# Performance work log

Hardware: AMD Instinct MI355X
Metric: run time of the kernel (lower is better)

## Reference

```python
import jax, jax.numpy as jnp
import numpy as np

B, S, HID = 2, 2048, 2048
H, HKV, D = 16, 8, 128
RQ, RK, RV = 6, 2, 2
WINDOW = 1024
SOFTCAP = 50.0
SCALING = D ** -0.5
NEG_INF = -2.3819763e38  # gemma mask fill value (fp32 safe)


def _rope(x, cos, sin):
    # Gemma rotary: split last dim into two halves treated as (real, imag).
    d2 = x.shape[-1] // 2
    x1, x2 = x[..., :d2], x[..., d2:]
    return jnp.concatenate([x1 * cos - x2 * sin, x1 * sin + x2 * cos], axis=-1)


def setup_inputs() -> dict:
    key = jax.random.key(0)
    ks = jax.random.split(key, 8)
    hidden_states = jax.random.normal(ks[0], (B, S, HID), jnp.float32)
    w = 0.02
    W_A_q = jax.random.normal(ks[1], (HID, H * RQ), jnp.float32) * w
    W_B_q = jax.random.normal(ks[2], (HID, H * RQ * D), jnp.float32) * w
    W_A_k = jax.random.normal(ks[3], (HID, HKV * RK), jnp.float32) * w
    W_B_k = jax.random.normal(ks[4], (HID, RK * D), jnp.float32) * w
    W_A_v = jax.random.normal(ks[5], (HID, HKV * RV), jnp.float32) * w
    W_B_v = jax.random.normal(ks[6], (HID, RV * D), jnp.float32) * w
    W_o = jax.random.normal(ks[7], (H * D, HID), jnp.float32) * w
    # rotary tables (theta=10000)
    pos = jnp.arange(S, dtype=jnp.float32)
    inv = 1.0 / (10000.0 ** (jnp.arange(0, D, 2, dtype=jnp.float32) / D))
    ang = pos[:, None] * inv[None, :]  # [S, D/2]
    freqs_cos, freqs_sin = jnp.cos(ang), jnp.sin(ang)
    # causal + sliding-window additive mask [B,1,S,S]
    i = jnp.arange(S)[:, None]
    j = jnp.arange(S)[None, :]
    allowed = (j <= i) & (i - j < WINDOW)
    mask = jnp.where(allowed, 0.0, NEG_INF).astype(jnp.float32)
    mask = jnp.broadcast_to(mask[None, None], (B, 1, S, S))
    kv_write_indices = jnp.arange(S, dtype=jnp.int32)  # prefill: identity write
    return {
        'hidden_states': hidden_states, 'W_A_q': W_A_q, 'W_B_q': W_B_q,
        'W_A_k': W_A_k, 'W_B_k': W_B_k, 'W_A_v': W_A_v, 'W_B_v': W_B_v,
        'W_o': W_o, 'freqs_cos': freqs_cos, 'freqs_sin': freqs_sin,
        'mask': mask, 'kv_write_indices': kv_write_indices,
    }


def reference(hidden_states, W_A_q, W_B_q, W_A_k, W_B_k, W_A_v, W_B_v, W_o,
              freqs_cos, freqs_sin, mask, kv_write_indices):
    # Prefill: kv_write_indices == arange(S); factorized cache == current factors.
    b, s, _ = hidden_states.shape
    Aq = (hidden_states @ W_A_q).reshape(b, s, H, RQ)       # [b,s,H,Rq]
    Bq = (hidden_states @ W_B_q).reshape(b, s, H, RQ, D)    # [b,s,H,Rq,d]
    Ak = (hidden_states @ W_A_k).reshape(b, s, HKV, RK)
    Bk = (hidden_states @ W_B_k).reshape(b, s, RK, D)
    Av = (hidden_states @ W_A_v).reshape(b, s, HKV, RV)
    Bv = (hidden_states @ W_B_v).reshape(b, s, RV, D)
    # RoPE on the B factors (as in the original: applied to B_q rows and B_k rows)
    Bq = _rope(Bq, freqs_cos[:, None, None, :], freqs_sin[:, None, None, :])
    Bk = _rope(Bk, freqs_cos[:, None, :], freqs_sin[:, None, :])
    # Contract rank factors. Identical math to the per-head
    # einsum('bqrd,bksd->bqkrs') + einsum('bqr,bks,bqkrs->bqk') since the
    # bilinear form factorizes: sum_{r,s} Aq_r Ak_s <Bq_r, Bk_s> = <q, k>.
    q = jnp.einsum('bshr,bshrd->bshd', Aq, Bq)               # [b,s,H,d]
    k = jnp.einsum('bsgr,bsrd->bsgd', Ak, Bk)                # [b,s,Hkv,d]
    v = jnp.einsum('bsgr,bsrd->bsgd', Av, Bv)
    rep = H // HKV
    k = jnp.repeat(k, rep, axis=2)                            # GQA expand
    v = jnp.repeat(v, rep, axis=2)
    scores = jnp.einsum('bqhd,bkhd->bhqk', q, k) * SCALING
    scores = jnp.tanh(scores / SOFTCAP) * SOFTCAP             # logit softcap
    scores = scores + mask                                    # local sliding mask
    probs = jax.nn.softmax(scores, axis=-1)
    out = jnp.einsum('bhqk,bkhd->bqhd', probs, v).reshape(b, s, H * D)
    return out @ W_o
```

## Files before the change

### kernel.cpp

```cpp
#include <hip/hip_runtime.h>
#include <hip/hip_bf16.h>

#define S_LEN 2048
#define HID 2048
#define NB 2
#define NH 16
#define NKV 8
#define DH 128
#define RQ 6
#define KG 2048
#define SCALING 0.08838834764831845f

typedef __attribute__((ext_vector_type(8))) short s16x8;
typedef __attribute__((ext_vector_type(4))) float f32x4;

__device__ __forceinline__ float bf2f(ushort u) {
    union { unsigned int i; float f; } v; v.i = ((unsigned int)u) << 16; return v.f;
}
__device__ __forceinline__ ushort f2bf(float f) {
    __hip_bfloat16 h = __float2bfloat16(f);
    return *reinterpret_cast<ushort*>(&h);
}
__device__ __forceinline__ void g2lds16(const void* g, void* l) {
    __builtin_amdgcn_global_load_lds((const __attribute__((address_space(1))) void*)g,
                                     (__attribute__((address_space(3))) void*)l, 16, 0, 0);
}

__global__ void k_prep(const float* __restrict__ hs, const float* __restrict__ WAq,
                       const float* __restrict__ WAk, const float* __restrict__ WAv,
                       const float* __restrict__ WBk, const float* __restrict__ WBv,
                       const float* __restrict__ WBq, const float* __restrict__ Wo,
                       ushort* __restrict__ Xb, ushort* __restrict__ WtS,
                       ushort* __restrict__ WtBq, ushort* __restrict__ WtWo) {
    __shared__ ushort tile[64][68];
    int idx = blockIdx.x;
    int t = threadIdx.x;
    if (idx < 2048) {
#pragma unroll
        for (int j = 0; j < 4; ++j) {
            int i = idx * 1024 + t + j * 256;
            float4 v = ((const float4*)hs)[i];
            ushort4 o;
            o.x = f2bf(v.x); o.y = f2bf(v.y); o.z = f2bf(v.z); o.w = f2bf(v.w);
            ((ushort4*)Xb)[i] = o;
        }
        return;
    }
    idx -= 2048;
    const float* in; ushort* out; int Nin, rowOff;
    if (idx < 64)        { in = WAq; out = WtS;  Nin = 96;    rowOff = 0; }
    else if (idx < 96)   { idx -= 64;   in = WAk; out = WtS;  Nin = 16;    rowOff = 96; }
    else if (idx < 128)  { idx -= 96;   in = WAv; out = WtS;  Nin = 16;    rowOff = 112; }
    else if (idx < 256)  { idx -= 128;  in = WBk; out = WtS;  Nin = 256;   rowOff = 128; }
    else if (idx < 384)  { idx -= 256;  in = WBv; out = WtS;  Nin = 256;   rowOff = 384; }
    else if (idx < 6528) { idx -= 384;  in = WBq; out = WtBq; Nin = 12288; rowOff = 0; }
    else                 { idx -= 6528; in = Wo;  out = WtWo; Nin = 2048;  rowOff = 0; }
    int k0 = (idx & 31) * 64, n0 = (idx >> 5) * 64;
#pragma unroll
    for (int i = 0; i < 4; ++i) {
        int f = t + i * 256;
        int r = f >> 4;
        int c = (f & 15) * 4;
        int nn = n0 + c;
        float4 v = make_float4(0.f, 0.f, 0.f, 0.f);
        if (nn < Nin) v = *(const float4*)&in[(size_t)(k0 + r) * Nin + nn];
        ushort4 u;
        u.x = f2bf(v.x); u.y = f2bf(v.y); u.z = f2bf(v.z); u.w = f2bf(v.w);
        *(ushort4*)&tile[r][c] = u;
    }
    __syncthreads();
#pragma unroll
    for (int i = 0; i < 4; ++i) {
        int f = t + i * 256;
        int nr = f >> 4;
        int kc = (f & 15) * 4;
        int nn = n0 + nr;
        if (nn < Nin) {
            ushort4 u;
            u.x = tile[kc][nr]; u.y = tile[kc + 1][nr];
            u.z = tile[kc + 2][nr]; u.w = tile[kc + 3][nr];
            *(ushort4*)&out[(size_t)(rowOff + nn) * KG + k0 + kc] = u;
        }
    }
}

__device__ __forceinline__ void stc(float* p, float v) { *p = v; }
__device__ __forceinline__ void stc(ushort* p, float v) { *p = f2bf(v); }

template<typename OutT>
__global__ __launch_bounds__(256, 2) void k_gemm(const ushort* __restrict__ A,
                                                 const ushort* __restrict__ Bt,
                                                 OutT* __restrict__ C, int ldc) {
    __shared__ ushort lA[128 * 64];
    __shared__ ushort lB[128 * 64];
    const int tid = threadIdx.x;
    const int l = tid & 63, w = tid >> 6;
    const int gx = gridDim.x;
    int flat = blockIdx.y * gx + blockIdx.x;
    const int nwg = gx * gridDim.y;
    if ((nwg & 7) == 0) {
        int qq = nwg >> 3;
        flat = (flat & 7) * qq + (flat >> 3);
    }
    const int m0 = (flat % gx) * 128, n0 = (flat / gx) * 128;
    const int wm = w >> 1, wn = w & 1;
    f32x4 acc[4][4] = {};
    const int swz = 16 * ((tid & 7) ^ ((tid >> 3) & 7));
    const int rowbase = tid >> 3;

    for (int k0 = 0; k0 < KG; k0 += 64) {
#pragma unroll
        for (int i = 0; i < 4; ++i) {
            int row = rowbase + i * 32;
            const char* srcA = (const char*)A + (((size_t)(m0 + row) * KG + k0) * 2) + swz;
            g2lds16(srcA, (char*)lA + tid * 16 + i * 4096);
            const char* srcB = (const char*)Bt + (((size_t)(n0 + row) * KG + k0) * 2) + swz;
            g2lds16(srcB, (char*)lB + tid * 16 + i * 4096);
        }
        __syncthreads();
#pragma unroll
        for (int kk = 0; kk < 2; ++kk) {
            s16x8 af[4], bfr[4];
            const int kb = kk * 64 + (l >> 4) * 16;
#pragma unroll
            for (int mf = 0; mf < 4; ++mf) {
                int row = wm * 64 + mf * 16 + (l & 15);
                af[mf] = *(const s16x8*)((const char*)lA + row * 128 + (kb ^ ((row & 7) << 4)));
            }
#pragma unroll
            for (int nf = 0; nf < 4; ++nf) {
                int row = wn * 64 + nf * 16 + (l & 15);
                bfr[nf] = *(const s16x8*)((const char*)lB + row * 128 + (kb ^ ((row & 7) << 4)));
            }
#pragma unroll
            for (int mf = 0; mf < 4; ++mf)
#pragma unroll
                for (int nf = 0; nf < 4; ++nf)
                    acc[mf][nf] = __builtin_amdgcn_mfma_f32_16x16x32_bf16(af[mf], bfr[nf], acc[mf][nf], 0, 0, 0);
        }
        __syncthreads();
    }
#pragma unroll
    for (int mf = 0; mf < 4; ++mf)
#pragma unroll
        for (int r = 0; r < 4; ++r) {
            int row = m0 + wm * 64 + mf * 16 + (l >> 4) * 4 + r;
#pragma unroll
            for (int nf = 0; nf < 4; ++nf) {
                int col = n0 + wn * 64 + nf * 16 + (l & 15);
                stc(C + (size_t)row * ldc + col, acc[mf][nf][r]);
            }
        }
}

__global__ __launch_bounds__(512, 2) void k_mega(const ushort* __restrict__ Xb,
                                                 const ushort* __restrict__ WtBq,
                                                 ushort* __restrict__ BqC,
                                                 const ushort* __restrict__ WtS,
                                                 float* __restrict__ Small) {
    __shared__ char sB[131072];
    const int tid = threadIdx.x;
    const int l = tid & 63, wid = tid >> 6;

    if (blockIdx.x < 768) {
        const ushort* A = Xb;
        const ushort* Bt = WtBq;
        ushort* C = BqC;
        const int ldc = 12288;
        const int wr = wid >> 2, wc = wid & 3;

        int flat = blockIdx.x;
        {
            int qq = 768 >> 3;
            flat = (flat & 7) * qq + (flat >> 3);
        }
        const int m0 = (flat & 15) * 256;
        const int n0 = (flat >> 4) * 256;

        const int rb = tid >> 3;
        const int swz = 16 * ((tid & 7) ^ (rb & 7));
        const char* pAh[2][2];
        const char* pBh[2][2];
#pragma unroll
        for (int h = 0; h < 2; ++h)
#pragma unroll
            for (int j = 0; j < 2; ++j) {
                pAh[h][j] = (const char*)A + (size_t)(m0 + j * 128 + h * 64 + rb) * (KG * 2) + swz;
                pBh[h][j] = (const char*)Bt + (size_t)(n0 + (j * 2 + (tid >> 8)) * 64 + h * 32 + (rb & 31)) * (KG * 2) + swz;
            }

        f32x4 acc[8][4] = {};
        s16x8 af[4][2], bf[4][2];

        const int arow = (l & 15) * 128;
        const int kxor0 = (0 * 64 + (l >> 4) * 16) ^ ((l & 7) << 4);
        const int kxor1 = (1 * 64 + (l >> 4) * 16) ^ ((l & 7) << 4);

#define STG_A(T, D, H)                                                                     \
    do {                                                                                   \
        g2lds16(pAh[H][0] + (size_t)(T) * 128, sB + (D) * 65536 + (H) * 16384 + tid * 16); \
        g2lds16(pAh[H][1] + (size_t)(T) * 128, sB + (D) * 65536 + (H) * 16384 + 8192 + tid * 16); \
    } while (0)
#define STG_B(T, D, H)                                                                     \
    do {                                                                                   \
        g2lds16(pBh[H][0] + (size_t)(T) * 128, sB + (D) * 65536 + 32768 + (H) * 16384 + tid * 16); \
        g2lds16(pBh[H][1] + (size_t)(T) * 128, sB + (D) * 65536 + 32768 + (H) * 16384 + 8192 + tid * 16); \
    } while (0)
#define RD_A(D, MH)                                                                        \
    do {                                                                                   \
        const char* ab = sB + (D) * 65536 + (MH) * 16384 + wr * 8192;                      \
        _Pragma("unroll") for (int mi = 0; mi < 4; ++mi) {                                 \
            af[mi][0] = *(const s16x8*)(ab + mi * 2048 + arow + kxor0);                    \
            af[mi][1] = *(const s16x8*)(ab + mi * 2048 + arow + kxor1);                    \
        }                                                                                  \
    } while (0)
#define RD_B(D, BH)                                                                        \
    do {                                                                                   \
        const char* bb = sB + (D) * 65536 + 32768 + (BH) * 16384 + wc * 4096;              \
        _Pragma("unroll") for (int ni = 0; ni < 2; ++ni) {                                 \
            bf[(BH) * 2 + ni][0] = *(const s16x8*)(bb + ni * 2048 + arow + kxor0);         \
            bf[(BH) * 2 + ni][1] = *(const s16x8*)(bb + ni * 2048 + arow + kxor1);         \
        }                                                                                  \
    } while (0)
#define QMFMA(MQ, NQ)                                                                      \
    do {                                                                                   \
        __builtin_amdgcn_s_setprio(1);                                                     \
        _Pragma("unroll") for (int mi = 0; mi < 4; ++mi)                                   \
        _Pragma("unroll") for (int ni = 0; ni < 2; ++ni)                                   \
        _Pragma("unroll") for (int k2 = 0; k2 < 2; ++k2)                                   \
            acc[(MQ) * 4 + mi][(NQ) * 2 + ni] = __builtin_amdgcn_mfma_f32_16x16x32_bf16(   \
                af[mi][k2], bf[(NQ) * 2 + ni][k2], acc[(MQ) * 4 + mi][(NQ) * 2 + ni], 0, 0, 0); \
        __builtin_amdgcn_s_setprio(0);                                                     \
    } while (0)
#define BAR()                                   \
    do {                                        \
        asm volatile("" ::: "memory");          \
        __builtin_amdgcn_s_barrier();           \
        asm volatile("" ::: "memory");          \
    } while (0)
#define VM6() asm volatile("s_waitcnt vmcnt(6)" ::: "memory")
#define VM0() asm volatile("s_waitcnt vmcnt(0)" ::: "memory")

        STG_A(0, 0, 0); STG_A(0, 0, 1); STG_B(0, 0, 0); STG_B(0, 0, 1);
        STG_B(1, 1, 0); STG_B(1, 1, 1); STG_A(1, 1, 0);
        VM6();
        BAR();

        for (int i = 0; i < 16; ++i) {
            const bool last = (i == 15);
            const int t1 = 2 * i + 1, t2 = 2 * i + 2, t3 = 2 * i + 3;
            RD_A(0, 0); RD_B(0, 0);
            STG_A(t1, 1, 1);
            BAR(); QMFMA(0, 0); BAR();
            RD_B(0, 1);
            if (!last) STG_A(t2, 0, 0);
            BAR(); QMFMA(0, 1); BAR();
            RD_A(0, 1);
            if (!last) STG_B(t2, 0, 0);
            BAR(); QMFMA(1, 1); BAR();
            if (!last) { STG_B(t2, 0, 1); VM6(); } else { VM0(); }
            BAR(); QMFMA(1, 0); BAR();
            RD_A(1, 0); RD_B(1, 0);
            if (!last) STG_A(t2, 0, 1);
            BAR(); QMFMA(0, 0); BAR();
            RD_B(1, 1);
            if (!last) STG_B(t3, 1, 0);
            BAR(); QMFMA(0, 1); BAR();
            RD_A(1, 1);
            if (!last) STG_B(t3, 1, 1);
            BAR(); QMFMA(1, 1); BAR();
            if (!last) { STG_A(t3, 1, 0); VM6(); }
            BAR(); QMFMA(1, 0); BAR();
        }

#undef STG_A
#undef STG_B
#undef RD_A
#undef RD_B
#undef QMFMA
#undef BAR
#undef VM6
#undef VM0

#pragma unroll
        for (int mf = 0; mf < 8; ++mf)
#pragma unroll
            for (int r = 0; r < 4; ++r) {
                int row = m0 + wr * 128 + mf * 16 + (l >> 4) * 4 + r;
#pragma unroll
                for (int nf = 0; nf < 4; ++nf) {
                    int col = n0 + wc * 64 + nf * 16 + (l & 15);
                    C[(size_t)row * ldc + col] = f2bf(acc[mf][nf][r]);
                }
            }
    } else {
        ushort* lA = (ushort*)sB;
        ushort* lB = (ushort*)(sB + 16384);
        int flat = blockIdx.x - 768;
        {
            int qq = 160 >> 3;
            flat = (flat & 7) * qq + (flat >> 3);
        }
        const int m0 = (flat % 32) * 128, n0 = (flat / 32) * 128;
        const int w = wid;
        const int wm = (w & 3) >> 1, wn = w & 1;
        f32x4 acc[4][4] = {};
        const int swz = 16 * ((tid & 7) ^ ((tid >> 3) & 7));
        const int rowbase = tid >> 3;

        for (int k0 = 0; k0 < KG; k0 += 64) {
#pragma unroll
            for (int i = 0; i < 2; ++i) {
                int row = rowbase + i * 64;
                const char* srcA = (const char*)Xb + (((size_t)(m0 + row) * KG + k0) * 2) + swz;
                g2lds16(srcA, (char*)lA + tid * 16 + i * 8192);
                const char* srcB = (const char*)WtS + (((size_t)(n0 + row) * KG + k0) * 2) + swz;
                g2lds16(srcB, (char*)lB + tid * 16 + i * 8192);
            }
            __syncthreads();
            if (w < 4) {
#pragma unroll
                for (int kk = 0; kk < 2; ++kk) {
                    s16x8 af[4], bfr[4];
                    const int kb = kk * 64 + (l >> 4) * 16;
#pragma unroll
                    for (int mf = 0; mf < 4; ++mf) {
                        int row = wm * 64 + mf * 16 + (l & 15);
                        af[mf] = *(const s16x8*)((const char*)lA + row * 128 + (kb ^ ((row & 7) << 4)));
                    }
#pragma unroll
                    for (int nf = 0; nf < 4; ++nf) {
                        int row = wn * 64 + nf * 16 + (l & 15);
                        bfr[nf] = *(const s16x8*)((const char*)lB + row * 128 + (kb ^ ((row & 7) << 4)));
                    }
#pragma unroll
                    for (int mf = 0; mf < 4; ++mf)
#pragma unroll
                        for (int nf = 0; nf < 4; ++nf)
                            acc[mf][nf] = __builtin_amdgcn_mfma_f32_16x16x32_bf16(af[mf], bfr[nf], acc[mf][nf], 0, 0, 0);
                }
            }
            __syncthreads();
        }
        if (w < 4) {
#pragma unroll
            for (int mf = 0; mf < 4; ++mf)
#pragma unroll
                for (int r = 0; r < 4; ++r) {
                    int row = m0 + wm * 64 + mf * 16 + (l >> 4) * 4 + r;
#pragma unroll
                    for (int nf = 0; nf < 4; ++nf) {
                        int col = n0 + wn * 64 + nf * 16 + (l & 15);
                        Small[(size_t)row * 640 + col] = acc[mf][nf][r];
                    }
                }
        }
    }
}

__global__ __launch_bounds__(512, 2) void k_gemm8(const ushort* __restrict__ A,
                                                  const ushort* __restrict__ Bt,
                                                  ushort* __restrict__ C, int ldc) {
    __shared__ char sB[131072];
    const int tid = threadIdx.x;
    const int l = tid & 63, wid = tid >> 6;
    const int wr = wid >> 2, wc = wid & 3;

    int flat = blockIdx.x;
    const int nwg = gridDim.x;
    if ((nwg & 7) == 0) {
        int qq = nwg >> 3;
        flat = (flat & 7) * qq + (flat >> 3);
    }
    const int m0 = (flat & 15) * 256;
    const int n0 = (flat >> 4) * 256;

    const int rb = tid >> 3;
    const int swz = 16 * ((tid & 7) ^ (rb & 7));
    const char* pAh[2][2];
    const char* pBh[2][2];
#pragma unroll
    for (int h = 0; h < 2; ++h)
#pragma unroll
        for (int j = 0; j < 2; ++j) {
            pAh[h][j] = (const char*)A + (size_t)(m0 + j * 128 + h * 64 + rb) * (KG * 2) + swz;
            pBh[h][j] = (const char*)Bt + (size_t)(n0 + (j * 2 + (tid >> 8)) * 64 + h * 32 + (rb & 31)) * (KG * 2) + swz;
        }

    f32x4 acc[8][4] = {};
    s16x8 af[4][2], bf[4][2];

    const int arow = (l & 15) * 128;
    const int kxor0 = (0 * 64 + (l >> 4) * 16) ^ ((l & 7) << 4);
    const int kxor1 = (1 * 64 + (l >> 4) * 16) ^ ((l & 7) << 4);

#define STG_A(T, D, H)                                                                     \
    do {                                                                                   \
        g2lds16(pAh[H][0] + (size_t)(T) * 128, sB + (D) * 65536 + (H) * 16384 + tid * 16); \
        g2lds16(pAh[H][1] + (size_t)(T) * 128, sB + (D) * 65536 + (H) * 16384 + 8192 + tid * 16); \
    } while (0)
#define STG_B(T, D, H)                                                                     \
    do {                                                                                   \
        g2lds16(pBh[H][0] + (size_t)(T) * 128, sB + (D) * 65536 + 32768 + (H) * 16384 + tid * 16); \
        g2lds16(pBh[H][1] + (size_t)(T) * 128, sB + (D) * 65536 + 32768 + (H) * 16384 + 8192 + tid * 16); \
    } while (0)
#define RD_A(D, MH)                                                                        \
    do {                                                                                   \
        const char* ab = sB + (D) * 65536 + (MH) * 16384 + wr * 8192;                      \
        _Pragma("unroll") for (int mi = 0; mi < 4; ++mi) {                                 \
            af[mi][0] = *(const s16x8*)(ab + mi * 2048 + arow + kxor0);                    \
            af[mi][1] = *(const s16x8*)(ab + mi * 2048 + arow + kxor1);                    \
        }                                                                                  \
    } while (0)
#define RD_B(D, BH)                                                                        \
    do {                                                                                   \
        const char* bb = sB + (D) * 65536 + 32768 + (BH) * 16384 + wc * 4096;              \
        _Pragma("unroll") for (int ni = 0; ni < 2; ++ni) {                                 \
            bf[(BH) * 2 + ni][0] = *(const s16x8*)(bb + ni * 2048 + arow + kxor0);         \
            bf[(BH) * 2 + ni][1] = *(const s16x8*)(bb + ni * 2048 + arow + kxor1);         \
        }                                                                                  \
    } while (0)
#define QMFMA(MQ, NQ)                                                                      \
    do {                                                                                   \
        __builtin_amdgcn_s_setprio(1);                                                     \
        _Pragma("unroll") for (int mi = 0; mi < 4; ++mi)                                   \
        _Pragma("unroll") for (int ni = 0; ni < 2; ++ni)                                   \
        _Pragma("unroll") for (int k2 = 0; k2 < 2; ++k2)                                   \
            acc[(MQ) * 4 + mi][(NQ) * 2 + ni] = __builtin_amdgcn_mfma_f32_16x16x32_bf16(   \
                af[mi][k2], bf[(NQ) * 2 + ni][k2], acc[(MQ) * 4 + mi][(NQ) * 2 + ni], 0, 0, 0); \
        __builtin_amdgcn_s_setprio(0);                                                     \
    } while (0)
#define BAR()                                   \
    do {                                        \
        asm volatile("" ::: "memory");          \
        __builtin_amdgcn_s_barrier();           \
        asm volatile("" ::: "memory");          \
    } while (0)
#define VM6() asm volatile("s_waitcnt vmcnt(6)" ::: "memory")
#define VM0() asm volatile("s_waitcnt vmcnt(0)" ::: "memory")

    STG_A(0, 0, 0); STG_A(0, 0, 1); STG_B(0, 0, 0); STG_B(0, 0, 1);
    STG_B(1, 1, 0); STG_B(1, 1, 1); STG_A(1, 1, 0);
    VM6();
    BAR();

    for (int i = 0; i < 16; ++i) {
        const bool last = (i == 15);
        const int t1 = 2 * i + 1, t2 = 2 * i + 2, t3 = 2 * i + 3;
        RD_A(0, 0); RD_B(0, 0);
        STG_A(t1, 1, 1);
        BAR(); QMFMA(0, 0); BAR();
        RD_B(0, 1);
        if (!last) STG_A(t2, 0, 0);
        BAR(); QMFMA(0, 1); BAR();
        RD_A(0, 1);
        if (!last) STG_B(t2, 0, 0);
        BAR(); QMFMA(1, 1); BAR();
        if (!last) { STG_B(t2, 0, 1); VM6(); } else { VM0(); }
        BAR(); QMFMA(1, 0); BAR();
        RD_A(1, 0); RD_B(1, 0);
        if (!last) STG_A(t2, 0, 1);
        BAR(); QMFMA(0, 0); BAR();
        RD_B(1, 1);
        if (!last) STG_B(t3, 1, 0);
        BAR(); QMFMA(0, 1); BAR();
        RD_A(1, 1);
        if (!last) STG_B(t3, 1, 1);
        BAR(); QMFMA(1, 1); BAR();
        if (!last) { STG_A(t3, 1, 0); VM6(); }
        BAR(); QMFMA(1, 0); BAR();
    }

#undef STG_A
#undef STG_B
#undef RD_A
#undef RD_B
#undef QMFMA

#pragma unroll
    for (int mf = 0; mf < 8; ++mf)
#pragma unroll
        for (int r = 0; r < 4; ++r) {
            int row = m0 + wr * 128 + mf * 16 + (l >> 4) * 4 + r;
#pragma unroll
            for (int nf = 0; nf < 4; ++nf) {
                int col = n0 + wc * 64 + nf * 16 + (l & 15);
                C[(size_t)row * ldc + col] = f2bf(acc[mf][nf][r]);
            }
        }
#undef BAR
#undef VM6
#undef VM0
}

__global__ __launch_bounds__(512, 2) void k_gemm8h(const ushort* __restrict__ A,
                                                   const ushort* __restrict__ Bt,
                                                   float* __restrict__ C, int ldc) {
    __shared__ char sB[98304];
    const int tid = threadIdx.x;
    const int l = tid & 63, wid = tid >> 6;
    const int wr = wid >> 2, wc = wid & 3;

    int flat = blockIdx.x;
    const int nwg = gridDim.x;
    if ((nwg & 7) == 0) {
        int qq = nwg >> 3;
        flat = (flat & 7) * qq + (flat >> 3);
    }
    const int m0 = (flat & 31) * 128;
    const int n0 = (flat >> 5) * 256;

    const int rb = tid >> 3;
    const int swz = 16 * ((tid & 7) ^ (rb & 7));
    const char* pA_[2];
    const char* pB_[2][2];
#pragma unroll
    for (int h = 0; h < 2; ++h) {
        pA_[h] = (const char*)A + (size_t)(m0 + (tid >> 8) * 64 + h * 32 + (rb & 31)) * (KG * 2) + swz;
#pragma unroll
        for (int j = 0; j < 2; ++j)
            pB_[h][j] = (const char*)Bt + (size_t)(n0 + (j * 2 + (tid >> 8)) * 64 + h * 32 + (rb & 31)) * (KG * 2) + swz;
    }

    f32x4 acc[4][4] = {};
    s16x8 af[2][2], bf[4][2];

    const int arow = (l & 15) * 128;
    const int kxor0 = ((l >> 4) * 16) ^ ((l & 7) << 4);
    const int kxor1 = (64 + (l >> 4) * 16) ^ ((l & 7) << 4);

#define STG_AH(T, D, H)                                                                    \
    g2lds16(pA_[H] + (size_t)(T) * 128, sB + (D) * 49152 + (H) * 8192 + tid * 16)
#define STG_BH(T, D, H)                                                                    \
    do {                                                                                   \
        g2lds16(pB_[H][0] + (size_t)(T) * 128, sB + (D) * 49152 + 16384 + (H) * 16384 + tid * 16); \
        g2lds16(pB_[H][1] + (size_t)(T) * 128, sB + (D) * 49152 + 16384 + (H) * 16384 + 8192 + tid * 16); \
    } while (0)
#define RD_AH(D, MH)                                                                       \
    do {                                                                                   \
        const char* ab = sB + (D) * 49152 + (MH) * 8192 + wr * 4096;                       \
        _Pragma("unroll") for (int mi = 0; mi < 2; ++mi) {                                 \
            af[mi][0] = *(const s16x8*)(ab + mi * 2048 + arow + kxor0);                    \
            af[mi][1] = *(const s16x8*)(ab + mi * 2048 + arow + kxor1);                    \
        }                                                                                  \
    } while (0)
#define RD_BH(D, BH)                                                                       \
    do {                                                                                   \
        const char* bb = sB + (D) * 49152 + 16384 + (BH) * 16384 + wc * 4096;              \
        _Pragma("unroll") for (int ni = 0; ni < 2; ++ni) {                                 \
            bf[(BH) * 2 + ni][0] = *(const s16x8*)(bb + ni * 2048 + arow + kxor0);         \
            bf[(BH) * 2 + ni][1] = *(const s16x8*)(bb + ni * 2048 + arow + kxor1);         \
        }                                                                                  \
    } while (0)
#define QMFMAH(MQ, NQ)                                                                     \
    do {                                                                                   \
        __builtin_amdgcn_s_setprio(1);                                                     \
        _Pragma("unroll") for (int mi = 0; mi < 2; ++mi)                                   \
        _Pragma("unroll") for (int ni = 0; ni < 2; ++ni)                                   \
        _Pragma("unroll") for (int k2 = 0; k2 < 2; ++k2)                                   \
            acc[(MQ) * 2 + mi][(NQ) * 2 + ni] = __builtin_amdgcn_mfma_f32_16x16x32_bf16(   \
                af[mi][k2], bf[(NQ) * 2 + ni][k2], acc[(MQ) * 2 + mi][(NQ) * 2 + ni], 0, 0, 0); \
        __builtin_amdgcn_s_setprio(0);                                                     \
    } while (0)
#define BAR()                                   \
    do {                                        \
        asm volatile("" ::: "memory");          \
        __builtin_amdgcn_s_barrier();           \
        asm volatile("" ::: "memory");          \
    } while (0)
#define VM5() asm volatile("s_waitcnt vmcnt(5)" ::: "memory")
#define VM0() asm volatile("s_waitcnt vmcnt(0)" ::: "memory")

    STG_AH(0, 0, 0); STG_AH(0, 0, 1); STG_BH(0, 0, 0); STG_BH(0, 0, 1);
    STG_BH(1, 1, 0); STG_BH(1, 1, 1); STG_AH(1, 1, 0);
    VM5();
    BAR();

    for (int i = 0; i < 16; ++i) {
        const bool last = (i == 15);
        const int t1 = 2 * i + 1, t2 = 2 * i + 2, t3 = 2 * i + 3;
        RD_AH(0, 0); RD_BH(0, 0);
        STG_AH(t1, 1, 1);
        BAR(); QMFMAH(0, 0); BAR();
        RD_BH(0, 1);
        if (!last) STG_AH(t2, 0, 0);
        BAR(); QMFMAH(0, 1); BAR();
        RD_AH(0, 1);
        if (!last) STG_BH(t2, 0, 0);
        BAR(); QMFMAH(1, 1); BAR();
        if (!last) { STG_BH(t2, 0, 1); VM5(); } else { VM0(); }
        BAR(); QMFMAH(1, 0); BAR();
        RD_AH(1, 0); RD_BH(1, 0);
        if (!last) STG_AH(t2, 0, 1);
        BAR(); QMFMAH(0, 0); BAR();
        RD_BH(1, 1);
        if (!last) STG_BH(t3, 1, 0);
        BAR(); QMFMAH(0, 1); BAR();
        RD_AH(1, 1);
        if (!last) STG_BH(t3, 1, 1);
        BAR(); QMFMAH(1, 1); BAR();
        if (!last) { STG_AH(t3, 1, 0); VM5(); }
        BAR(); QMFMAH(1, 0); BAR();
    }

#undef STG_AH
#undef STG_BH
#undef RD_AH
#undef RD_BH
#undef QMFMAH
#undef BAR
#undef VM5
#undef VM0

#pragma unroll
    for (int a = 0; a < 4; ++a)
#pragma unroll
        for (int r = 0; r < 4; ++r) {
            int row = m0 + wr * 64 + a * 16 + (l >> 4) * 4 + r;
#pragma unroll
            for (int b2 = 0; b2 < 4; ++b2) {
                int col = n0 + wc * 64 + b2 * 16 + (l & 15);
                C[(size_t)row * ldc + col] = acc[a][b2][r];
            }
        }
}

__global__ void k_contract_q(const ushort* __restrict__ bq, const float* __restrict__ small,
                             const float* __restrict__ cosT, const float* __restrict__ sinT,
                             ushort* __restrict__ q, int pitch, int hbase) {
    int srow = blockIdx.x;
    int b = srow >> 11, sl = srow & 2047;
    int t = threadIdx.x;
    int l = t & 63;
    int hloc = blockIdx.y * 4 + (t >> 6);
    int h = hbase + hloc;
    const ushort* bqr = bq + (size_t)srow * pitch + hloc * 768;
    const float* af = small + (size_t)srow * 640 + h * RQ;
    float y0 = 0.f, y1 = 0.f;
#pragma unroll
    for (int r = 0; r < RQ; ++r) {
        float a = af[r];
        ushort2 v = *(const ushort2*)&bqr[r * 128 + 2 * l];
        y0 += a * bf2f(v.x);
        y1 += a * bf2f(v.y);
    }
    float z0 = __shfl_xor(y0, 32);
    float z1 = __shfl_xor(y1, 32);
    int d = (l & 31) * 2;
    float2 cs = *(const float2*)&cosT[sl * 64 + d];
    float2 sn = *(const float2*)&sinT[sl * 64 + d];
    size_t o = ((size_t)(b * NH + h) * S_LEN + sl) * DH;
    ushort2 outv;
    if (l < 32) {
        outv.x = f2bf((y0 * cs.x - z0 * sn.x) * SCALING);
        outv.y = f2bf((y1 * cs.y - z1 * sn.y) * SCALING);
        *(ushort2*)&q[o + d] = outv;
    } else {
        outv.x = f2bf((z0 * sn.x + y0 * cs.x) * SCALING);
        outv.y = f2bf((z1 * sn.y + y1 * cs.y) * SCALING);
        *(ushort2*)&q[o + 64 + d] = outv;
    }
}

__global__ void k_contract_kv(const float* __restrict__ small, const float* __restrict__ cosT,
                              const float* __restrict__ sinT, ushort* __restrict__ kk,
                              ushort* __restrict__ vT) {
    int srow = blockIdx.x;
    int b = srow >> 11, sl = srow & 2047;
    int t = threadIdx.x;
    int d2 = t & 63, g = t >> 6;
    const float* row = small + (size_t)srow * 640;
    float k1 = 0.f, k2 = 0.f, v1 = 0.f, v2 = 0.f;
#pragma unroll
    for (int r = 0; r < 2; ++r) {
        float ak = row[96 + g * 2 + r];
        k1 += ak * row[128 + r * 128 + d2];
        k2 += ak * row[128 + r * 128 + 64 + d2];
        float av = row[112 + g * 2 + r];
        v1 += av * row[384 + r * 128 + d2];
        v2 += av * row[384 + r * 128 + 64 + d2];
    }
    float c = cosT[sl * 64 + d2], s = sinT[sl * 64 + d2];
    float kr1 = k1 * c - k2 * s, kr2 = k1 * s + k2 * c;
    size_t ko = ((size_t)(b * NKV + g) * S_LEN + sl) * DH + d2;
    kk[ko] = f2bf(kr1);
    kk[ko + 64] = f2bf(kr2);
    size_t vo = ((size_t)(b * NKV + g) * DH + d2) * S_LEN + sl;
    vT[vo] = f2bf(v1);
    vT[vo + (size_t)64 * S_LEN] = f2bf(v2);
}

__device__ __forceinline__ float softcap_p(float x) {
    float z = x * 0.02f;
    float z2 = z * z;
    float num = z * fmaf(z2, z2 + 105.f, 945.f);
    float den = fmaf(z2, fmaf(z2, 15.f, 420.f), 945.f);
    return __expf(fmaf(50.f, __fdividef(num, den), -50.f));
}

template<int FUSEQ>
__global__ __launch_bounds__(512, 2) void k_attn(const ushort* __restrict__ qsrc,
                                                 const float* __restrict__ small,
                                                 const float* __restrict__ cosT,
                                                 const float* __restrict__ sinT,
                                                 const ushort* __restrict__ kk,
                                                 const ushort* __restrict__ vT,
                                                 ushort* __restrict__ O) {
    __shared__ char sK[2][16384];
    __shared__ char sV[2][16384];
    __shared__ char sP[16384];
    const int f = blockIdx.x;
    const int xcd = f & 7;
    const int j = f >> 3;
    const int bg = xcd * 2 + (j >> 5);
    const int qb = 31 - (j & 31);
    const int b = bg >> 3, g = bg & 7;
    const int tid = threadIdx.x, l = tid & 63, w = tid >> 6;
    const int w4 = w & 3;
    const int h = g * 2 + (w >> 2);
    const int qs = qb * 64;
    const int q0 = qs + w4 * 16;

    s16x8 qf[4];
    if (FUSEQ) {
        const int row = q0 + (l & 15);
        const int srow = b * S_LEN + row;
        const float* af = small + (size_t)srow * 640 + h * RQ;
        const ushort* bqr = qsrc + (size_t)srow * 12288 + h * 768;
        const int k8 = (l >> 4) * 8;
#pragma unroll
        for (int grp = 0; grp < 2; ++grp) {
            const int dbase = grp * 32 + k8;
            float x1[8] = {}, x2[8] = {};
#pragma unroll
            for (int r = 0; r < RQ; ++r) {
                float a = af[r];
                s16x8 v1 = *(const s16x8*)&bqr[r * 128 + dbase];
                s16x8 v2 = *(const s16x8*)&bqr[r * 128 + 64 + dbase];
#pragma unroll
                for (int e = 0; e < 8; ++e) {
                    x1[e] = fmaf(a, bf2f((ushort)v1[e]), x1[e]);
                    x2[e] = fmaf(a, bf2f((ushort)v2[e]), x2[e]);
                }
            }
            const float* cp = &cosT[row * 64 + dbase];
            const float* sp = &sinT[row * 64 + dbase];
            s16x8 lo, hi;
#pragma unroll
            for (int e = 0; e < 8; ++e) {
                float c = cp[e], s = sp[e];
                lo[e] = (short)f2bf((x1[e] * c - x2[e] * s) * SCALING);
                hi[e] = (short)f2bf((x1[e] * s + x2[e] * c) * SCALING);
            }
            qf[grp] = lo;
            qf[grp + 2] = hi;
        }
    } else {
        const ushort* qbase = qsrc + ((size_t)(b * NH + h) * S_LEN) * DH;
        const char* qrow = (const char*)(qbase + (size_t)(q0 + (l & 15)) * DH);
#pragma unroll
        for (int ds = 0; ds < 4; ++ds)
            qf[ds] = *(const s16x8*)(qrow + ds * 64 + (l >> 4) * 16);
    }

    f32x4 acc[8] = {};
    float lrow[4] = {0.f, 0.f, 0.f, 0.f};

    const size_t kgbase = ((size_t)(b * NKV + g) * S_LEN) * DH * 2;
    const size_t vgbase = ((size_t)(b * NKV + g) * DH) * S_LEN * 2;

    const int jt0 = (qs > 1023) ? ((qs - 1023) >> 6) : 0;
    const int ibase = q0 + (l >> 4) * 4;

    const int krow0 = tid >> 4, kcolb = (tid & 15) * 16;
    const int vrow0 = tid >> 3, vcolb = (tid & 7) * 16;

#define STAGE_KV(JT, SLOT)                                                                   \
    do {                                                                                     \
        _Pragma("unroll")                                                                    \
        for (int i = 0; i < 2; ++i) {                                                        \
            int row = krow0 + i * 32;                                                        \
            const char* src = (const char*)kk + kgbase + ((size_t)((JT) * 64 + row)) * 256   \
                              + (kcolb ^ ((row & 7) << 4));                                  \
            g2lds16(src, &sK[SLOT][tid * 16 + i * 8192]);                                    \
        }                                                                                    \
        _Pragma("unroll")                                                                    \
        for (int i = 0; i < 2; ++i) {                                                        \
            int row = vrow0 + i * 64;                                                        \
            const char* src = (const char*)vT + vgbase + (size_t)row * 4096                  \
                              + (size_t)(JT) * 128 + (vcolb ^ ((row & 7) << 4));             \
            g2lds16(src, &sV[SLOT][tid * 16 + i * 8192]);                                    \
        }                                                                                    \
    } while (0)

    STAGE_KV(jt0, 0);
    asm volatile("s_waitcnt vmcnt(0)" ::: "memory");
    __builtin_amdgcn_s_barrier();
    asm volatile("" ::: "memory");

    for (int jt = jt0; jt <= qb; ++jt) {
        const int cur = (jt - jt0) & 1;
        if (jt < qb) STAGE_KV(jt + 1, cur ^ 1);

        const bool diag = (jt == qb);
        const bool wclip = (jt == jt0) && (qs > 1023);

        f32x4 sc[4] = {};
#pragma unroll
        for (int ct = 0; ct < 4; ++ct) {
            if (diag && ct > w4) continue;
            f32x4 z = {};
            int row = ct * 16 + (l & 15);
#pragma unroll
            for (int ds = 0; ds < 4; ++ds) {
                int kb = ds * 64 + (l >> 4) * 16;
                s16x8 kf = *(const s16x8*)(&sK[cur][row * 256 + (kb ^ ((row & 7) << 4))]);
                z = __builtin_amdgcn_mfma_f32_16x16x32_bf16(qf[ds], kf, z, 0, 0, 0);
            }
            sc[ct] = z;
        }
        float p[4][4];
        if (!diag && !wclip) {
#pragma unroll
            for (int ct = 0; ct < 4; ++ct)
#pragma unroll
                for (int r = 0; r < 4; ++r) {
                    float pe = softcap_p(sc[ct][r]);
                    p[ct][r] = pe;
                    lrow[r] += pe;
                }
        } else if (diag) {
#pragma unroll
            for (int ct = 0; ct < 4; ++ct) {
                if (ct > w4) {
#pragma unroll
                    for (int r = 0; r < 4; ++r) p[ct][r] = 0.f;
                    continue;
                }
                int j2 = jt * 64 + ct * 16 + (l & 15);
#pragma unroll
                for (int r = 0; r < 4; ++r) {
                    float pe = softcap_p(sc[ct][r]);
                    pe = (j2 <= ibase + r) ? pe : 0.f;
                    p[ct][r] = pe;
                    lrow[r] += pe;
                }
            }
        } else {
#pragma unroll
            for (int ct = 0; ct < 4; ++ct) {
                int j2 = jt * 64 + ct * 16 + (l & 15);
#pragma unroll
                for (int r = 0; r < 4; ++r) {
                    float pe = softcap_p(sc[ct][r]);
                    pe = (j2 > ibase + r - 1024) ? pe : 0.f;
                    p[ct][r] = pe;
                    lrow[r] += pe;
                }
            }
        }
#pragma unroll
        for (int ct = 0; ct < 4; ++ct) {
            int col = ct * 16 + (l & 15);
#pragma unroll
            for (int r = 0; r < 4; ++r) {
                int row = (l >> 4) * 4 + r;
                *(ushort*)(sP + w * 2048 + row * 128 + ((col * 2) ^ ((row & 7) << 4))) = f2bf(p[ct][r]);
            }
        }
#pragma unroll
        for (int s2 = 0; s2 < 2; ++s2) {
            int rowp = l & 15;
            int kb = s2 * 64 + (l >> 4) * 16;
            s16x8 pf = *(const s16x8*)(sP + w * 2048 + rowp * 128 + (kb ^ ((rowp & 7) << 4)));
#pragma unroll
            for (int dt = 0; dt < 8; ++dt) {
                int d = dt * 16 + (l & 15);
                s16x8 vf = *(const s16x8*)(&sV[cur][d * 128 + (kb ^ ((d & 7) << 4))]);
                acc[dt] = __builtin_amdgcn_mfma_f32_16x16x32_bf16(pf, vf, acc[dt], 0, 0, 0);
            }
        }

        asm volatile("s_waitcnt vmcnt(0)" ::: "memory");
        __builtin_amdgcn_s_barrier();
        asm volatile("" ::: "memory");
    }
#undef STAGE_KV

#pragma unroll
    for (int r = 0; r < 4; ++r) {
        float rs = lrow[r];
        rs += __shfl_xor(rs, 1); rs += __shfl_xor(rs, 2);
        rs += __shfl_xor(rs, 4); rs += __shfl_xor(rs, 8);
        lrow[r] = rs;
    }
#pragma unroll
    for (int r = 0; r < 4; ++r) {
        int row = qs + w4 * 16 + (l >> 4) * 4 + r;
        float inv = 1.f / lrow[r];
#pragma unroll
        for (int dt = 0; dt < 8; ++dt)
            O[((size_t)(b * S_LEN + row)) * HID + h * DH + dt * 16 + (l & 15)] = f2bf(acc[dt][r] * inv);
    }
}

extern "C" void kernel_launch(void* const* d_in, const int* in_sizes, int n_in,
                              void* d_out, int out_size, void* d_ws, size_t ws_size,
                              hipStream_t stream) {
    (void)in_sizes; (void)n_in; (void)out_size;
    const float* hs  = (const float*)d_in[0];
    const float* WAq = (const float*)d_in[1];
    const float* WBq = (const float*)d_in[2];
    const float* WAk = (const float*)d_in[3];
    const float* WBk = (const float*)d_in[4];
    const float* WAv = (const float*)d_in[5];
    const float* WBv = (const float*)d_in[6];
    const float* Wo  = (const float*)d_in[7];
    const float* fc  = (const float*)d_in[8];
    const float* fs  = (const float*)d_in[9];

    char* ws = (char*)d_ws;
    ushort* Xb    = (ushort*)(ws + 0);
    ushort* WtS   = (ushort*)(ws + 16777216);
    ushort* WtBq  = (ushort*)(ws + 19398656);
    ushort* WtWo  = (ushort*)(ws + 69730304);
    float*  Small = (float*) (ws + 78118912);
    ushort* BqC   = (ushort*)(ws + 88604672);

    const bool bigws = (ws_size >= 239599616ull);
    size_t tail = bigws ? 189267968ull : 113770496ull;
    ushort* qB  = (ushort*)(ws + tail);
    ushort* kB  = (ushort*)(ws + tail + 16777216);
    ushort* vTB = (ushort*)(ws + tail + 25165824);
    ushort* OB  = (ushort*)(ws + tail + 33554432);

    k_prep<<<9600, 256, 0, stream>>>(hs, WAq, WAk, WAv, WBk, WBv, WBq, Wo,
                                     Xb, WtS, WtBq, WtWo);

    if (bigws) {
        k_mega<<<928, 512, 0, stream>>>(Xb, WtBq, BqC, WtS, Small);
        k_contract_kv<<<4096, 512, 0, stream>>>(Small, fc, fs, kB, vTB);
        k_attn<1><<<512, 512, 0, stream>>>(BqC, Small, fc, fs, kB, vTB, OB);
    } else {
        k_gemm<float><<<dim3(32, 5), 256, 0, stream>>>(Xb, WtS, Small, 640);
        k_contract_kv<<<4096, 512, 0, stream>>>(Small, fc, fs, kB, vTB);
        for (int c = 0; c < 4; ++c) {
            k_gemm8<<<192, 512, 0, stream>>>(Xb, WtBq + (size_t)c * 3072 * KG, BqC, 3072);
            k_contract_q<<<dim3(4096, 1), 256, 0, stream>>>(BqC, Small, fc, fs, qB, 3072, c * 4);
        }
        k_attn<0><<<512, 512, 0, stream>>>(qB, Small, fc, fs, kB, vTB, OB);
    }

    k_gemm8h<<<256, 512, 0, stream>>>(OB, WtWo, (float*)d_out, 2048);
}
```

Measured before the change: 418.9 us.

## Split attention blocks per head and drop KV double buffering

Each attention block now handles a single query head with 4 waves (256 threads) instead of both GQA heads with 8 waves, and twice as many blocks are launched. The K/V double buffer is removed: each iteration loads its tile into one LDS buffer, then synchronizes, computes, and synchronizes again. The smaller LDS footprint may let more blocks fit per CU, but the two heads that share a KV group now load their K/V tiles separately, and loads no longer overlap compute within a block.

Result: faster. 401.1 us (-4.2%).

```diff
diff --git a/kernel.cpp b/kernel.cpp
--- a/kernel.cpp
+++ b/kernel.cpp
@@ -699,27 +699,28 @@
 }
 
 template<int FUSEQ>
-__global__ __launch_bounds__(512, 2) void k_attn(const ushort* __restrict__ qsrc,
+__global__ __launch_bounds__(256, 2) void k_attn(const ushort* __restrict__ qsrc,
                                                  const float* __restrict__ small,
                                                  const float* __restrict__ cosT,
                                                  const float* __restrict__ sinT,
                                                  const ushort* __restrict__ kk,
                                                  const ushort* __restrict__ vT,
                                                  ushort* __restrict__ O) {
-    __shared__ char sK[2][16384];
-    __shared__ char sV[2][16384];
-    __shared__ char sP[16384];
+    __shared__ char sK[16384];
+    __shared__ char sV[16384];
+    __shared__ char sP[8192];
     const int f = blockIdx.x;
     const int xcd = f & 7;
     const int j = f >> 3;
-    const int bg = xcd * 2 + (j >> 5);
-    const int qb = 31 - (j & 31);
+    const int bg = xcd * 2 + (j >> 6);
+    const int rem = j & 63;
+    const int qb = 31 - (rem >> 1);
+    const int hh = rem & 1;
     const int b = bg >> 3, g = bg & 7;
+    const int h = g * 2 + hh;
     const int tid = threadIdx.x, l = tid & 63, w = tid >> 6;
-    const int w4 = w & 3;
-    const int h = g * 2 + (w >> 2);
     const int qs = qb * 64;
-    const int q0 = qs + w4 * 16;
+    const int q0 = qs + w * 16;
 
     s16x8 qf[4];
     if (FUSEQ) {
@@ -772,35 +773,22 @@
     const int jt0 = (qs > 1023) ? ((qs - 1023) >> 6) : 0;
     const int ibase = q0 + (l >> 4) * 4;
 
-    const int krow0 = tid >> 4, kcolb = (tid & 15) * 16;
-    const int vrow0 = tid >> 3, vcolb = (tid & 7) * 16;
-
-#define STAGE_KV(JT, SLOT)                                                                   \
-    do {                                                                                     \
-        _Pragma("unroll")                                                                    \
-        for (int i = 0; i < 2; ++i) {                                                        \
-            int row = krow0 + i * 32;                                                        \
-            const char* src = (const char*)kk + kgbase + ((size_t)((JT) * 64 + row)) * 256   \
-                              + (kcolb ^ ((row & 7) << 4));                                  \
-            g2lds16(src, &sK[SLOT][tid * 16 + i * 8192]);                                    \
-        }                                                                                    \
-        _Pragma("unroll")                                                                    \
-        for (int i = 0; i < 2; ++i) {                                                        \
-            int row = vrow0 + i * 64;                                                        \
-            const char* src = (const char*)vT + vgbase + (size_t)row * 4096                  \
-                              + (size_t)(JT) * 128 + (vcolb ^ ((row & 7) << 4));             \
-            g2lds16(src, &sV[SLOT][tid * 16 + i * 8192]);                                    \
-        }                                                                                    \
-    } while (0)
-
-    STAGE_KV(jt0, 0);
-    asm volatile("s_waitcnt vmcnt(0)" ::: "memory");
-    __builtin_amdgcn_s_barrier();
-    asm volatile("" ::: "memory");
-
     for (int jt = jt0; jt <= qb; ++jt) {
-        const int cur = (jt - jt0) & 1;
-        if (jt < qb) STAGE_KV(jt + 1, cur ^ 1);
+#pragma unroll
+        for (int i = 0; i < 4; ++i) {
+            int row = (tid >> 4) + i * 16;
+            int colb = (tid & 15) * 16;
+            const char* src = (const char*)kk + kgbase + ((size_t)(jt * 64 + row)) * 256 + (colb ^ ((row & 7) << 4));
+            g2lds16(src, sK + tid * 16 + i * 4096);
+        }
+#pragma unroll
+        for (int i = 0; i < 4; ++i) {
+            int row = (tid >> 3) + i * 32;
+            int colb = (tid & 7) * 16;
+            const char* src = (const char*)vT + vgbase + (size_t)row * 4096 + (size_t)jt * 128 + (colb ^ ((row & 7) << 4));
+            g2lds16(src, sV + tid * 16 + i * 4096);
+        }
+        __syncthreads();
 
         const bool diag = (jt == qb);
         const bool wclip = (jt == jt0) && (qs > 1023);
@@ -808,13 +796,13 @@
         f32x4 sc[4] = {};
 #pragma unroll
         for (int ct = 0; ct < 4; ++ct) {
-            if (diag && ct > w4) continue;
+            if (diag && ct > w) continue;
             f32x4 z = {};
             int row = ct * 16 + (l & 15);
 #pragma unroll
             for (int ds = 0; ds < 4; ++ds) {
                 int kb = ds * 64 + (l >> 4) * 16;
-                s16x8 kf = *(const s16x8*)(&sK[cur][row * 256 + (kb ^ ((row & 7) << 4))]);
+                s16x8 kf = *(const s16x8*)(sK + row * 256 + (kb ^ ((row & 7) << 4)));
                 z = __builtin_amdgcn_mfma_f32_16x16x32_bf16(qf[ds], kf, z, 0, 0, 0);
             }
             sc[ct] = z;
@@ -832,7 +820,7 @@
         } else if (diag) {
 #pragma unroll
             for (int ct = 0; ct < 4; ++ct) {
-                if (ct > w4) {
+                if (ct > w) {
 #pragma unroll
                     for (int r = 0; r < 4; ++r) p[ct][r] = 0.f;
                     continue;
@@ -876,17 +864,12 @@
 #pragma unroll
             for (int dt = 0; dt < 8; ++dt) {
                 int d = dt * 16 + (l & 15);
-                s16x8 vf = *(const s16x8*)(&sV[cur][d * 128 + (kb ^ ((d & 7) << 4))]);
+                s16x8 vf = *(const s16x8*)(sV + d * 128 + (kb ^ ((d & 7) << 4)));
                 acc[dt] = __builtin_amdgcn_mfma_f32_16x16x32_bf16(pf, vf, acc[dt], 0, 0, 0);
             }
         }
-
-        asm volatile("s_waitcnt vmcnt(0)" ::: "memory");
-        __builtin_amdgcn_s_barrier();
-        asm volatile("" ::: "memory");
-    }
-#undef STAGE_KV
-
+        __syncthreads();
+    }
 #pragma unroll
     for (int r = 0; r < 4; ++r) {
         float rs = lrow[r];
@@ -896,7 +879,7 @@
     }
 #pragma unroll
     for (int r = 0; r < 4; ++r) {
-        int row = qs + w4 * 16 + (l >> 4) * 4 + r;
+        int row = qs + w * 16 + (l >> 4) * 4 + r;
         float inv = 1.f / lrow[r];
 #pragma unroll
         for (int dt = 0; dt < 8; ++dt)
@@ -940,7 +923,7 @@
     if (bigws) {
         k_mega<<<928, 512, 0, stream>>>(Xb, WtBq, BqC, WtS, Small);
         k_contract_kv<<<4096, 512, 0, stream>>>(Small, fc, fs, kB, vTB);
-        k_attn<1><<<512, 512, 0, stream>>>(BqC, Small, fc, fs, kB, vTB, OB);
+        k_attn<1><<<1024, 256, 0, stream>>>(BqC, Small, fc, fs, kB, vTB, OB);
     } else {
         k_gemm<float><<<dim3(32, 5), 256, 0, stream>>>(Xb, WtS, Small, 640);
         k_contract_kv<<<4096, 512, 0, stream>>>(Small, fc, fs, kB, vTB);
@@ -948,7 +931,7 @@
             k_gemm8<<<192, 512, 0, stream>>>(Xb, WtBq + (size_t)c * 3072 * KG, BqC, 3072);
             k_contract_q<<<dim3(4096, 1), 256, 0, stream>>>(BqC, Small, fc, fs, qB, 3072, c * 4);
         }
-        k_attn<0><<<512, 512, 0, stream>>>(qB, Small, fc, fs, kB, vTB, OB);
+        k_attn<0><<<1024, 256, 0, stream>>>(qB, Small, fc, fs, kB, vTB, OB);
     }
 
     k_gemm8h<<<256, 512, 0, stream>>>(OB, WtWo, (float*)d_out, 2048);
```
